# Kernel tuning notes

Measured on AMD Instinct MI355X. Metric: run time of the kernel, lower is better.

Reference implementation:

```python
import jax, jax.numpy as jnp
import numpy as np

B, N, E, H = 2, 2048, 256, 4
DK = E // H


def setup_inputs() -> dict:
    key = jax.random.key(0)
    ks = jax.random.split(key, 7)
    xav = lambda k, shape, fan_in, fan_out: jax.random.uniform(
        k, shape, minval=-1.0, maxval=1.0, dtype=jnp.float32
    ) * np.sqrt(6.0 / (fan_in + fan_out))
    return {
        "node_embeddings": jax.random.normal(ks[0], (B, N, E), dtype=jnp.float32),
        "adjacency_matrices": jax.random.randint(ks[1], (B, N, N), 0, 2, dtype=jnp.int32),
        "Wq": xav(ks[2], (H, E, DK), E, DK),
        "Wk": xav(ks[3], (H, E, DK), E, DK),
        "Wv": xav(ks[4], (H, E, DK), E, DK),
        "Wo": xav(ks[5], (E, E), E, E),
        "bo": jnp.zeros((E,), dtype=jnp.float32),
    }


def reference(node_embeddings, adjacency_matrices, Wq, Wk, Wv, Wo, bo):
    # Per-head projections: (B,N,E) x (H,E,dk) -> (B,H,N,dk)
    Q = jnp.einsum("bnd,hde->bhne", node_embeddings, Wq)
    K = jnp.einsum("bnd,hde->bhne", node_embeddings, Wk)
    V = jnp.einsum("bnd,hde->bhne", node_embeddings, Wv)
    scale = 1.0 / np.sqrt(DK).astype(np.float32)
    # (B,H,N,N) scores, adjacency-masked
    scores = jnp.einsum("bhne,bhme->bhnm", Q, K) * scale
    mask = adjacency_matrices[:, None, :, :] > 0  # (B,1,N,N) -> broadcast over H
    scores = jnp.where(mask, scores, -jnp.inf)
    attn = jax.nn.softmax(scores, axis=-1)
    heads = jnp.einsum("bhnm,bhme->bhne", attn, V)  # (B,H,N,dk)
    concat = heads.transpose(0, 2, 1, 3).reshape(node_embeddings.shape[0], node_embeddings.shape[1], E)
    return concat @ Wo.T + bo
```

## Files before the change

### kernel.cpp

```cpp
#include <hip/hip_runtime.h>
#include <hip/hip_bf16.h>
#include <math.h>

#define Bb 2
#define Nn 2048
#define Ee 256
#define Hh 4
#define DKk 64

typedef __bf16 bf16x8 __attribute__((ext_vector_type(8)));
typedef float f32x4 __attribute__((ext_vector_type(4)));

#define QSCALE 0.18033688011112042f
#define MOFF 20.0f

__global__ void __launch_bounds__(256) pack_fused(
        const int* __restrict__ adj,
        unsigned long long* __restrict__ bits,
        const float* __restrict__ x,
        const float* __restrict__ Wq,
        const float* __restrict__ Wk,
        const float* __restrict__ Wv,
        const float* __restrict__ Wo,
        __bf16* __restrict__ xb,
        __bf16* __restrict__ WB,
        __bf16* __restrict__ WoB) {
    int blk = blockIdx.x;
    int t = threadIdx.x;
    if (blk < 2048) {
        int wid = t >> 6, lane = t & 63;
        #pragma unroll
        for (int i = 0; i < 4; ++i) {
            int gid = blk * 16 + i * 4 + wid;
            int row = gid >> 3;
            int g = gid & 7;
            const int4* src = (const int4*)(adj + (size_t)row * Nn + g * 256) + lane;
            int4 v = *src;
            unsigned long long b0 = __ballot(v.x > 0);
            unsigned long long b1 = __ballot(v.y > 0);
            unsigned long long b2 = __ballot(v.z > 0);
            unsigned long long b3 = __ballot(v.w > 0);
            if (lane == 0) {
                ulonglong2* dst = (ulonglong2*)(bits + (size_t)gid * 4);
                ulonglong2 p0; p0.x = b0; p0.y = b1;
                ulonglong2 p1; p1.x = b2; p1.y = b3;
                dst[0] = p0;
                dst[1] = p1;
            }
        }
    } else {
        int b2 = blk - 2048;
        if (b2 < 1024) {
            size_t i = ((size_t)b2 * 256 + t) * 4;
            float4 v = *(const float4*)(x + i);
            __bf16 o[4] = {(__bf16)v.x, (__bf16)v.y, (__bf16)v.z, (__bf16)v.w};
            *(ushort4*)(xb + i) = *(ushort4*)o;
        } else if (b2 < 1024 + 768) {
            int row = b2 - 1024;
            int m = row >> 8, h = (row >> 6) & 3, e = row & 63;
            const float* W = (m == 0 ? Wq : (m == 1 ? Wk : Wv));
            float sc = (m == 0) ? QSCALE : 1.0f;
            WB[(size_t)row * 256 + t] = (__bf16)(W[h * 16384 + t * 64 + e] * sc);
        } else {
            int b3 = b2 - 1792;
            size_t i = ((size_t)b3 * 256 + t) * 4;
            float4 v = *(const float4*)(Wo + i);
            __bf16 o[4] = {(__bf16)v.x, (__bf16)v.y, (__bf16)v.z, (__bf16)v.w};
            *(ushort4*)(WoB + i) = *(ushort4*)o;
        }
    }
}

__global__ void __launch_bounds__(256) qkv_mfma(
        const __bf16* __restrict__ xb,
        const __bf16* __restrict__ WB,
        __bf16* __restrict__ Qb,
        __bf16* __restrict__ Kf,
        __bf16* __restrict__ Vf) {
    int blk = blockIdx.x;
    int bm = blk >> 1, half = blk & 1;
    int t = threadIdx.x;
    int wid = t >> 6, lane = t & 63, li = lane & 15, quad = lane >> 4;
    int row0 = bm * 16;

    bf16x8 a[8];
    const __bf16* ap = xb + (size_t)(row0 + li) * 256 + quad * 8;
    #pragma unroll
    for (int i = 0; i < 8; ++i) a[i] = *(const bf16x8*)(ap + i * 32);

    int b = row0 >> 11;
    int nloc = row0 & 2047;

    #pragma unroll 1
    for (int j = 0; j < 6; ++j) {
        int c0 = wid * 192 + half * 96 + j * 16;
        const __bf16* bp = WB + (size_t)(c0 + li) * 256 + quad * 8;
        f32x4 acc = (f32x4){0.f, 0.f, 0.f, 0.f};
        #pragma unroll
        for (int i = 0; i < 8; ++i) {
            bf16x8 bfrag = *(const bf16x8*)(bp + i * 32);
            acc = __builtin_amdgcn_mfma_f32_16x16x32_bf16(a[i], bfrag, acc, 0, 0, 0);
        }
        int m = c0 >> 8;
        int h = (c0 >> 6) & 3;
        int e0 = c0 & 63;
        int bh = b * 4 + h;
        if (m == 0) {
            size_t base = ((size_t)bh * Nn + nloc + quad * 4) * 64 + e0 + li;
            #pragma unroll
            for (int r = 0; r < 4; ++r) Qb[base + (size_t)r * 64] = (__bf16)acc[r];
        } else if (m == 1) {
            int e = e0 + li;
            int cp = e >> 5, ek = e & 31;
            int qA = ek >> 3, jA = ek & 7;
            int kt = nloc >> 4;
            size_t ub = (((size_t)(bh * 128 + kt)) * 2 + cp) * 512 + qA * 128 + jA;
            #pragma unroll
            for (int r = 0; r < 4; ++r) Kf[ub + (quad * 4 + r) * 8] = (__bf16)acc[r];
        } else {
            int e = e0 + li;
            int et = e >> 4, liA = e & 15;
            int key32 = nloc >> 5;
            int nnb = nloc & 16;
            size_t ub = (((size_t)(bh * 64 + key32)) * 4 + et) * 512 + liA * 8;
            #pragma unroll
            for (int r = 0; r < 4; ++r) {
                int nn = nnb + quad * 4 + r;
                Vf[ub + (nn >> 3) * 128 + (nn & 7)] = (__bf16)acc[r];
            }
        }
    }
}

__global__ void __launch_bounds__(256, 3) attn_kernel(
        const __bf16* __restrict__ Qb,
        const __bf16* __restrict__ Kf,
        const __bf16* __restrict__ Vf,
        const unsigned long long* __restrict__ bits,
        __bf16* __restrict__ heads) {
    __shared__ __align__(16) __bf16 PS[4][16][72];
    __shared__ float OL[4][16][68];
    __shared__ float lL[4][16];

    int blk = blockIdx.x;
    int bh = blk & 7, qt = blk >> 3;
    int b = bh >> 2, h = bh & 3;
    int t = threadIdx.x;
    int wid = t >> 6, lane = t & 63, li = lane & 15, quad = lane >> 4;
    int q0 = qt * 16;

    const __bf16* qp = Qb + ((size_t)bh * Nn + q0 + li) * 64 + quad * 8;
    bf16x8 qa0 = *(const bf16x8*)qp;
    bf16x8 qa1 = *(const bf16x8*)(qp + 32);

    f32x4 o[4];
    #pragma unroll
    for (int et = 0; et < 4; ++et) o[et] = (f32x4){0.f, 0.f, 0.f, 0.f};
    f32x4 ls = (f32x4){0.f, 0.f, 0.f, 0.f};

    const __bf16* Kfb = Kf + (size_t)bh * 131072;
    const __bf16* Vfb = Vf + (size_t)bh * 131072;
    int lanew = lane * 8;

    #pragma unroll 1
    for (int g = 0; g < 2; ++g) {
        int grp = wid * 2 + g;
        unsigned long long aw[4];
        #pragma unroll
        for (int r = 0; r < 4; ++r)
            aw[r] = bits[(((size_t)b * Nn + q0 + quad * 4 + r) * 8 + grp) * 4 + (li & 3)];

        #pragma unroll 1
        for (int tt = 0; tt < 4; ++tt) {
            int key64 = grp * 4 + tt;

            bf16x8 kb[4][2];
            #pragma unroll
            for (int nt = 0; nt < 4; ++nt)
                #pragma unroll
                for (int c = 0; c < 2; ++c)
                    kb[nt][c] = *(const bf16x8*)(Kfb + ((size_t)((key64 * 4 + nt) * 2 + c)) * 512 + lanew);
            bf16x8 vb[4][2];
            #pragma unroll
            for (int et = 0; et < 4; ++et)
                #pragma unroll
                for (int kc = 0; kc < 2; ++kc)
                    vb[et][kc] = *(const bf16x8*)(Vfb + ((size_t)((key64 * 2 + kc) * 4 + et)) * 512 + lanew);

            f32x4 s[4];
            __builtin_amdgcn_s_setprio(1);
            #pragma unroll
            for (int nt = 0; nt < 4; ++nt) {
                f32x4 z = (f32x4){-MOFF, -MOFF, -MOFF, -MOFF};
                z = __builtin_amdgcn_mfma_f32_16x16x32_bf16(qa0, kb[nt][0], z, 0, 0, 0);
                s[nt] = __builtin_amdgcn_mfma_f32_16x16x32_bf16(qa1, kb[nt][1], z, 0, 0, 0);
            }
            __builtin_amdgcn_s_setprio(0);

            int shb = tt * 16 + (li >> 2);
            unsigned awt[4];
            #pragma unroll
            for (int r = 0; r < 4; ++r) awt[r] = (unsigned)(aw[r] >> shb);

            #pragma unroll
            for (int nt = 0; nt < 4; ++nt) {
                #pragma unroll
                for (int r = 0; r < 4; ++r) {
                    unsigned bit = (awt[r] >> (nt * 4)) & 1u;
                    float p = bit ? __builtin_amdgcn_exp2f(s[nt][r]) : 0.f;
                    ls[r] += p;
                    PS[wid][quad * 4 + r][nt * 16 + li] = (__bf16)p;
                }
            }

            bf16x8 pa0 = *(const bf16x8*)&PS[wid][li][quad * 8];
            bf16x8 pa1 = *(const bf16x8*)&PS[wid][li][quad * 8 + 32];

            __builtin_amdgcn_s_setprio(1);
            #pragma unroll
            for (int et = 0; et < 4; ++et) {
                o[et] = __builtin_amdgcn_mfma_f32_16x16x32_bf16(pa0, vb[et][0], o[et], 0, 0, 0);
                o[et] = __builtin_amdgcn_mfma_f32_16x16x32_bf16(pa1, vb[et][1], o[et], 0, 0, 0);
            }
            __builtin_amdgcn_s_setprio(0);
        }
    }

    #pragma unroll
    for (int r = 0; r < 4; ++r) {
        float v = ls[r];
        v += __shfl_xor(v, 1, 64);
        v += __shfl_xor(v, 2, 64);
        v += __shfl_xor(v, 4, 64);
        v += __shfl_xor(v, 8, 64);
        if (li == 0) lL[wid][quad * 4 + r] = v;
        #pragma unroll
        for (int et = 0; et < 4; ++et)
            OL[wid][quad * 4 + r][et * 16 + li] = o[et][r];
    }
    __syncthreads();

    int qi = t >> 4, e0 = (t & 15) * 4;
    float l = lL[0][qi] + lL[1][qi] + lL[2][qi] + lL[3][qi];
    float inv = 1.0f / l;
    float s0 = 0.f, s1 = 0.f, s2 = 0.f, s3 = 0.f;
    #pragma unroll
    for (int w = 0; w < 4; ++w) {
        s0 += OL[w][qi][e0];
        s1 += OL[w][qi][e0 + 1];
        s2 += OL[w][qi][e0 + 2];
        s3 += OL[w][qi][e0 + 3];
    }
    __bf16 ob[4] = {(__bf16)(s0 * inv), (__bf16)(s1 * inv),
                    (__bf16)(s2 * inv), (__bf16)(s3 * inv)};
    __bf16* dst = heads + ((size_t)b * Nn + q0 + qi) * 256 + h * 64 + e0;
    *(ushort4*)dst = *(ushort4*)ob;
}

__global__ void __launch_bounds__(256) outproj_mfma(
        const __bf16* __restrict__ hb,
        const __bf16* __restrict__ WoB,
        const float* __restrict__ bo,
        float* __restrict__ out) {
    int blk = blockIdx.x;
    int bm = blk >> 1, half = blk & 1;
    int t = threadIdx.x;
    int wid = t >> 6, lane = t & 63, li = lane & 15, quad = lane >> 4;
    int row0 = bm * 16;

    bf16x8 a[8];
    const __bf16* ap = hb + (size_t)(row0 + li) * 256 + quad * 8;
    #pragma unroll
    for (int i = 0; i < 8; ++i) a[i] = *(const bf16x8*)(ap + i * 32);

    #pragma unroll 1
    for (int j = 0; j < 2; ++j) {
        int c0 = wid * 64 + half * 32 + j * 16;
        const __bf16* bp = WoB + (size_t)(c0 + li) * 256 + quad * 8;
        f32x4 acc = (f32x4){0.f, 0.f, 0.f, 0.f};
        #pragma unroll
        for (int i = 0; i < 8; ++i) {
            bf16x8 bfrag = *(const bf16x8*)(bp + i * 32);
            acc = __builtin_amdgcn_mfma_f32_16x16x32_bf16(a[i], bfrag, acc, 0, 0, 0);
        }
        int c = c0 + li;
        float bias = bo[c];
        size_t base = ((size_t)row0 + quad * 4) * 256 + c;
        #pragma unroll
        for (int r = 0; r < 4; ++r) out[base + (size_t)r * 256] = acc[r] + bias;
    }
}

extern "C" void kernel_launch(void* const* d_in, const int* in_sizes, int n_in,
                              void* d_out, int out_size, void* d_ws, size_t ws_size,
                              hipStream_t stream) {
    const float* x   = (const float*)d_in[0];
    const int*   adj = (const int*)d_in[1];
    const float* Wq  = (const float*)d_in[2];
    const float* Wk  = (const float*)d_in[3];
    const float* Wv  = (const float*)d_in[4];
    const float* Wo  = (const float*)d_in[5];
    const float* bo  = (const float*)d_in[6];
    float* out = (float*)d_out;

    char* ws = (char*)d_ws;
    const size_t MB = 1024 * 1024;
    __bf16* Qb  = (__bf16*)(ws);
    __bf16* Kf  = (__bf16*)(ws + 2 * MB);
    __bf16* Vf  = (__bf16*)(ws + 4 * MB);
    unsigned long long* bits = (unsigned long long*)(ws + 6 * MB);
    __bf16* xb  = (__bf16*)(ws + 7 * MB);
    __bf16* WB  = (__bf16*)(ws + 9 * MB);
    __bf16* WoB = (__bf16*)(ws + 9 * MB + 512 * 1024);
    __bf16* headsb = xb;

    pack_fused<<<3904, 256, 0, stream>>>(adj, bits, x, Wq, Wk, Wv, Wo, xb, WB, WoB);
    qkv_mfma<<<512, 256, 0, stream>>>(xb, WB, Qb, Kf, Vf);
    attn_kernel<<<Bb * Hh * (Nn / 16), 256, 0, stream>>>(Qb, Kf, Vf, bits, headsb);
    outproj_mfma<<<512, 256, 0, stream>>>(headsb, WoB, bo, out);
}
```

Baseline: 135.1 us.

## Process two 16-query tiles per attention block to reuse K/V loads

```diff
diff --git a/kernel.cpp b/kernel.cpp
--- a/kernel.cpp
+++ b/kernel.cpp
@@ -132,7 +132,7 @@
     }
 }
 
-__global__ void __launch_bounds__(256, 3) attn_kernel(
+__global__ void __launch_bounds__(256, 2) attn_kernel(
         const __bf16* __restrict__ Qb,
         const __bf16* __restrict__ Kf,
         const __bf16* __restrict__ Vf,
@@ -143,20 +143,28 @@
     __shared__ float lL[4][16];
 
     int blk = blockIdx.x;
-    int bh = blk & 7, qt = blk >> 3;
+    int bh = blk & 7, qp = blk >> 3;
     int b = bh >> 2, h = bh & 3;
     int t = threadIdx.x;
     int wid = t >> 6, lane = t & 63, li = lane & 15, quad = lane >> 4;
-    int q0 = qt * 16;
-
-    const __bf16* qp = Qb + ((size_t)bh * Nn + q0 + li) * 64 + quad * 8;
-    bf16x8 qa0 = *(const bf16x8*)qp;
-    bf16x8 qa1 = *(const bf16x8*)(qp + 32);
-
-    f32x4 o[4];
+    int q0 = qp * 32;
+
+    bf16x8 qa[2][2];
     #pragma unroll
-    for (int et = 0; et < 4; ++et) o[et] = (f32x4){0.f, 0.f, 0.f, 0.f};
-    f32x4 ls = (f32x4){0.f, 0.f, 0.f, 0.f};
+    for (int qq = 0; qq < 2; ++qq) {
+        const __bf16* qpp = Qb + ((size_t)bh * Nn + q0 + qq * 16 + li) * 64 + quad * 8;
+        qa[qq][0] = *(const bf16x8*)qpp;
+        qa[qq][1] = *(const bf16x8*)(qpp + 32);
+    }
+
+    f32x4 o[2][4];
+    #pragma unroll
+    for (int qq = 0; qq < 2; ++qq)
+        #pragma unroll
+        for (int et = 0; et < 4; ++et) o[qq][et] = (f32x4){0.f, 0.f, 0.f, 0.f};
+    f32x4 ls[2];
+    ls[0] = (f32x4){0.f, 0.f, 0.f, 0.f};
+    ls[1] = (f32x4){0.f, 0.f, 0.f, 0.f};
 
     const __bf16* Kfb = Kf + (size_t)bh * 131072;
     const __bf16* Vfb = Vf + (size_t)bh * 131072;
@@ -165,10 +173,12 @@
     #pragma unroll 1
     for (int g = 0; g < 2; ++g) {
         int grp = wid * 2 + g;
-        unsigned long long aw[4];
-        #pragma unroll
-        for (int r = 0; r < 4; ++r)
-            aw[r] = bits[(((size_t)b * Nn + q0 + quad * 4 + r) * 8 + grp) * 4 + (li & 3)];
+        unsigned long long aw[2][4];
+        #pragma unroll
+        for (int qq = 0; qq < 2; ++qq)
+            #pragma unroll
+            for (int r = 0; r < 4; ++r)
+                aw[qq][r] = bits[(((size_t)b * Nn + q0 + qq * 16 + quad * 4 + r) * 8 + grp) * 4 + (li & 3)];
 
         #pragma unroll 1
         for (int tt = 0; tt < 4; ++tt) {
@@ -187,74 +197,82 @@
                 for (int kc = 0; kc < 2; ++kc)
                     vb[et][kc] = *(const bf16x8*)(Vfb + ((size_t)((key64 * 2 + kc) * 4 + et)) * 512 + lanew);
 
-            f32x4 s[4];
-            __builtin_amdgcn_s_setprio(1);
-            #pragma unroll
-            for (int nt = 0; nt < 4; ++nt) {
-                f32x4 z = (f32x4){-MOFF, -MOFF, -MOFF, -MOFF};
-                z = __builtin_amdgcn_mfma_f32_16x16x32_bf16(qa0, kb[nt][0], z, 0, 0, 0);
-                s[nt] = __builtin_amdgcn_mfma_f32_16x16x32_bf16(qa1, kb[nt][1], z, 0, 0, 0);
+            int shb = tt * 16 + (li >> 2);
+
+            #pragma unroll
+            for (int qq = 0; qq < 2; ++qq) {
+                f32x4 s[4];
+                __builtin_amdgcn_s_setprio(1);
+                #pragma unroll
+                for (int nt = 0; nt < 4; ++nt) {
+                    f32x4 z = (f32x4){-MOFF, -MOFF, -MOFF, -MOFF};
+                    z = __builtin_amdgcn_mfma_f32_16x16x32_bf16(qa[qq][0], kb[nt][0], z, 0, 0, 0);
+                    s[nt] = __builtin_amdgcn_mfma_f32_16x16x32_bf16(qa[qq][1], kb[nt][1], z, 0, 0, 0);
+                }
+                __builtin_amdgcn_s_setprio(0);
+
+                unsigned awt[4];
+                #pragma unroll
+                for (int r = 0; r < 4; ++r) awt[r] = (unsigned)(aw[qq][r] >> shb);
+
+                #pragma unroll
+                for (int nt = 0; nt < 4; ++nt) {
+                    #pragma unroll
+                    for (int r = 0; r < 4; ++r) {
+                        unsigned bit = (awt[r] >> (nt * 4)) & 1u;
+                        float p = bit ? __builtin_amdgcn_exp2f(s[nt][r]) : 0.f;
+                        ls[qq][r] += p;
+                        PS[wid][quad * 4 + r][nt * 16 + li] = (__bf16)p;
+                    }
+                }
+
+                bf16x8 pa0 = *(const bf16x8*)&PS[wid][li][quad * 8];
+                bf16x8 pa1 = *(const bf16x8*)&PS[wid][li][quad * 8 + 32];
+
+                __builtin_amdgcn_s_setprio(1);
+                #pragma unroll
+                for (int et = 0; et < 4; ++et) {
+                    o[qq][et] = __builtin_amdgcn_mfma_f32_16x16x32_bf16(pa0, vb[et][0], o[qq][et], 0, 0, 0);
+                    o[qq][et] = __builtin_amdgcn_mfma_f32_16x16x32_bf16(pa1, vb[et][1], o[qq][et], 0, 0, 0);
+                }
+                __builtin_amdgcn_s_setprio(0);
             }
-            __builtin_amdgcn_s_setprio(0);
-
-            int shb = tt * 16 + (li >> 2);
-            unsigned awt[4];
-            #pragma unroll
-            for (int r = 0; r < 4; ++r) awt[r] = (unsigned)(aw[r] >> shb);
-
-            #pragma unroll
-            for (int nt = 0; nt < 4; ++nt) {
-                #pragma unroll
-                for (int r = 0; r < 4; ++r) {
-                    unsigned bit = (awt[r] >> (nt * 4)) & 1u;
-                    float p = bit ? __builtin_amdgcn_exp2f(s[nt][r]) : 0.f;
-                    ls[r] += p;
-                    PS[wid][quad * 4 + r][nt * 16 + li] = (__bf16)p;
-                }
-            }
-
-            bf16x8 pa0 = *(const bf16x8*)&PS[wid][li][quad * 8];
-            bf16x8 pa1 = *(const bf16x8*)&PS[wid][li][quad * 8 + 32];
-
-            __builtin_amdgcn_s_setprio(1);
-            #pragma unroll
-            for (int et = 0; et < 4; ++et) {
-                o[et] = __builtin_amdgcn_mfma_f32_16x16x32_bf16(pa0, vb[et][0], o[et], 0, 0, 0);
-                o[et] = __builtin_amdgcn_mfma_f32_16x16x32_bf16(pa1, vb[et][1], o[et], 0, 0, 0);
-            }
-            __builtin_amdgcn_s_setprio(0);
-        }
-    }
-
-    #pragma unroll
-    for (int r = 0; r < 4; ++r) {
-        float v = ls[r];
-        v += __shfl_xor(v, 1, 64);
-        v += __shfl_xor(v, 2, 64);
-        v += __shfl_xor(v, 4, 64);
-        v += __shfl_xor(v, 8, 64);
-        if (li == 0) lL[wid][quad * 4 + r] = v;
-        #pragma unroll
-        for (int et = 0; et < 4; ++et)
-            OL[wid][quad * 4 + r][et * 16 + li] = o[et][r];
-    }
-    __syncthreads();
-
-    int qi = t >> 4, e0 = (t & 15) * 4;
-    float l = lL[0][qi] + lL[1][qi] + lL[2][qi] + lL[3][qi];
-    float inv = 1.0f / l;
-    float s0 = 0.f, s1 = 0.f, s2 = 0.f, s3 = 0.f;
-    #pragma unroll
-    for (int w = 0; w < 4; ++w) {
-        s0 += OL[w][qi][e0];
-        s1 += OL[w][qi][e0 + 1];
-        s2 += OL[w][qi][e0 + 2];
-        s3 += OL[w][qi][e0 + 3];
-    }
-    __bf16 ob[4] = {(__bf16)(s0 * inv), (__bf16)(s1 * inv),
-                    (__bf16)(s2 * inv), (__bf16)(s3 * inv)};
-    __bf16* dst = heads + ((size_t)b * Nn + q0 + qi) * 256 + h * 64 + e0;
-    *(ushort4*)dst = *(ushort4*)ob;
+        }
+    }
+
+    #pragma unroll 1
+    for (int qq = 0; qq < 2; ++qq) {
+        #pragma unroll
+        for (int r = 0; r < 4; ++r) {
+            float v = ls[qq][r];
+            v += __shfl_xor(v, 1, 64);
+            v += __shfl_xor(v, 2, 64);
+            v += __shfl_xor(v, 4, 64);
+            v += __shfl_xor(v, 8, 64);
+            if (li == 0) lL[wid][quad * 4 + r] = v;
+            #pragma unroll
+            for (int et = 0; et < 4; ++et)
+                OL[wid][quad * 4 + r][et * 16 + li] = o[qq][et][r];
+        }
+        __syncthreads();
+
+        int qi = t >> 4, e0 = (t & 15) * 4;
+        float l = lL[0][qi] + lL[1][qi] + lL[2][qi] + lL[3][qi];
+        float inv = 1.0f / l;
+        float s0 = 0.f, s1 = 0.f, s2 = 0.f, s3 = 0.f;
+        #pragma unroll
+        for (int w = 0; w < 4; ++w) {
+            s0 += OL[w][qi][e0];
+            s1 += OL[w][qi][e0 + 1];
+            s2 += OL[w][qi][e0 + 2];
+            s3 += OL[w][qi][e0 + 3];
+        }
+        __bf16 ob[4] = {(__bf16)(s0 * inv), (__bf16)(s1 * inv),
+                        (__bf16)(s2 * inv), (__bf16)(s3 * inv)};
+        __bf16* dst = heads + ((size_t)b * Nn + q0 + qq * 16 + qi) * 256 + h * 64 + e0;
+        *(ushort4*)dst = *(ushort4*)ob;
+        __syncthreads();
+    }
 }
 
 __global__ void __launch_bounds__(256) outproj_mfma(
@@ -316,6 +334,6 @@
 
     pack_fused<<<3904, 256, 0, stream>>>(adj, bits, x, Wq, Wk, Wv, Wo, xb, WB, WoB);
     qkv_mfma<<<512, 256, 0, stream>>>(xb, WB, Qb, Kf, Vf);
-    attn_kernel<<<Bb * Hh * (Nn / 16), 256, 0, stream>>>(Qb, Kf, Vf, bits, headsb);
+    attn_kernel<<<512, 256, 0, stream>>>(Qb, Kf, Vf, bits, headsb);
     outproj_mfma<<<512, 256, 0, stream>>>(headsb, WoB, bo, out);
 }
```

After: 138.0 us. 2.1% more time.

## Fuse all four stages into one cooperative persistent kernel with grid syncs

Applied to the files above, without the earlier changes.

```diff
diff --git a/kernel.cpp b/kernel.cpp
--- a/kernel.cpp
+++ b/kernel.cpp
@@ -1,6 +1,8 @@
 #include <hip/hip_runtime.h>
+#include <hip/hip_cooperative_groups.h>
 #include <hip/hip_bf16.h>
-#include <math.h>
+
+namespace cg = cooperative_groups;
 
 #define Bb 2
 #define Nn 2048
@@ -14,7 +16,7 @@
 #define QSCALE 0.18033688011112042f
 #define MOFF 20.0f
 
-__global__ void __launch_bounds__(256) pack_fused(
+__global__ void __launch_bounds__(512) fused_all(
         const int* __restrict__ adj,
         unsigned long long* __restrict__ bits,
         const float* __restrict__ x,
@@ -22,16 +24,30 @@
         const float* __restrict__ Wk,
         const float* __restrict__ Wv,
         const float* __restrict__ Wo,
+        const float* __restrict__ bo,
         __bf16* __restrict__ xb,
         __bf16* __restrict__ WB,
-        __bf16* __restrict__ WoB) {
+        __bf16* __restrict__ WoB,
+        __bf16* __restrict__ Qb,
+        __bf16* __restrict__ Kf,
+        __bf16* __restrict__ Vf,
+        __bf16* __restrict__ heads,
+        float* __restrict__ out) {
+    cg::grid_group grid = cg::this_grid();
+
     int blk = blockIdx.x;
     int t = threadIdx.x;
-    if (blk < 2048) {
-        int wid = t >> 6, lane = t & 63;
-        #pragma unroll
-        for (int i = 0; i < 4; ++i) {
-            int gid = blk * 16 + i * 4 + wid;
+    int wid = t >> 6, lane = t & 63, li = lane & 15, quad = lane >> 4;
+    int w4 = wid & 3, sub = wid >> 2;
+
+    __shared__ __align__(16) __bf16 PS[8][16][72];
+    __shared__ float OL[8][16][68];
+    __shared__ float lL[8][16];
+
+    {
+        #pragma unroll 4
+        for (int i = 0; i < 16; ++i) {
+            int gid = blk * 128 + wid * 16 + i;
             int row = gid >> 3;
             int g = gid & 7;
             const int4* src = (const int4*)(adj + (size_t)row * Nn + g * 256) + lane;
@@ -48,246 +64,232 @@
                 dst[1] = p1;
             }
         }
-    } else {
-        int b2 = blk - 2048;
-        if (b2 < 1024) {
-            size_t i = ((size_t)b2 * 256 + t) * 4;
+        int tid = blk * 512 + t;
+        #pragma unroll
+        for (int j = 0; j < 2; ++j) {
+            size_t i = ((size_t)(tid + j * 131072)) * 4;
             float4 v = *(const float4*)(x + i);
-            __bf16 o[4] = {(__bf16)v.x, (__bf16)v.y, (__bf16)v.z, (__bf16)v.w};
-            *(ushort4*)(xb + i) = *(ushort4*)o;
-        } else if (b2 < 1024 + 768) {
-            int row = b2 - 1024;
-            int m = row >> 8, h = (row >> 6) & 3, e = row & 63;
-            const float* W = (m == 0 ? Wq : (m == 1 ? Wk : Wv));
-            float sc = (m == 0) ? QSCALE : 1.0f;
-            WB[(size_t)row * 256 + t] = (__bf16)(W[h * 16384 + t * 64 + e] * sc);
-        } else {
-            int b3 = b2 - 1792;
-            size_t i = ((size_t)b3 * 256 + t) * 4;
+            __bf16 o4[4] = {(__bf16)v.x, (__bf16)v.y, (__bf16)v.z, (__bf16)v.w};
+            *(ushort4*)(xb + i) = *(ushort4*)o4;
+        }
+        #pragma unroll
+        for (int j = 0; j < 2; ++j) {
+            int id = tid + j * 131072;
+            if (id < 196608) {
+                int row = id >> 8, col = id & 255;
+                int m = row >> 8, h = (row >> 6) & 3, e = row & 63;
+                const float* W = (m == 0 ? Wq : (m == 1 ? Wk : Wv));
+                float sc = (m == 0) ? QSCALE : 1.0f;
+                WB[(size_t)row * 256 + col] = (__bf16)(W[h * 16384 + col * 64 + e] * sc);
+            }
+        }
+        if (tid < 16384) {
+            size_t i = (size_t)tid * 4;
             float4 v = *(const float4*)(Wo + i);
-            __bf16 o[4] = {(__bf16)v.x, (__bf16)v.y, (__bf16)v.z, (__bf16)v.w};
-            *(ushort4*)(WoB + i) = *(ushort4*)o;
+            __bf16 o4[4] = {(__bf16)v.x, (__bf16)v.y, (__bf16)v.z, (__bf16)v.w};
+            *(ushort4*)(WoB + i) = *(ushort4*)o4;
         }
     }
-}
-
-__global__ void __launch_bounds__(256) qkv_mfma(
-        const __bf16* __restrict__ xb,
-        const __bf16* __restrict__ WB,
-        __bf16* __restrict__ Qb,
-        __bf16* __restrict__ Kf,
-        __bf16* __restrict__ Vf) {
-    int blk = blockIdx.x;
-    int bm = blk >> 1, half = blk & 1;
-    int t = threadIdx.x;
-    int wid = t >> 6, lane = t & 63, li = lane & 15, quad = lane >> 4;
-    int row0 = bm * 16;
-
-    bf16x8 a[8];
-    const __bf16* ap = xb + (size_t)(row0 + li) * 256 + quad * 8;
-    #pragma unroll
-    for (int i = 0; i < 8; ++i) a[i] = *(const bf16x8*)(ap + i * 32);
-
-    int b = row0 >> 11;
-    int nloc = row0 & 2047;
-
-    #pragma unroll 1
-    for (int j = 0; j < 6; ++j) {
-        int c0 = wid * 192 + half * 96 + j * 16;
-        const __bf16* bp = WB + (size_t)(c0 + li) * 256 + quad * 8;
-        f32x4 acc = (f32x4){0.f, 0.f, 0.f, 0.f};
+    __threadfence();
+    grid.sync();
+
+    {
+        int row0 = blk * 16;
+        bf16x8 a[8];
+        const __bf16* ap = xb + (size_t)(row0 + li) * 256 + quad * 8;
         #pragma unroll
-        for (int i = 0; i < 8; ++i) {
-            bf16x8 bfrag = *(const bf16x8*)(bp + i * 32);
-            acc = __builtin_amdgcn_mfma_f32_16x16x32_bf16(a[i], bfrag, acc, 0, 0, 0);
-        }
-        int m = c0 >> 8;
-        int h = (c0 >> 6) & 3;
-        int e0 = c0 & 63;
-        int bh = b * 4 + h;
-        if (m == 0) {
-            size_t base = ((size_t)bh * Nn + nloc + quad * 4) * 64 + e0 + li;
-            #pragma unroll
-            for (int r = 0; r < 4; ++r) Qb[base + (size_t)r * 64] = (__bf16)acc[r];
-        } else if (m == 1) {
-            int e = e0 + li;
-            int cp = e >> 5, ek = e & 31;
-            int qA = ek >> 3, jA = ek & 7;
-            int kt = nloc >> 4;
-            size_t ub = (((size_t)(bh * 128 + kt)) * 2 + cp) * 512 + qA * 128 + jA;
-            #pragma unroll
-            for (int r = 0; r < 4; ++r) Kf[ub + (quad * 4 + r) * 8] = (__bf16)acc[r];
-        } else {
-            int e = e0 + li;
-            int et = e >> 4, liA = e & 15;
-            int key32 = nloc >> 5;
-            int nnb = nloc & 16;
-            size_t ub = (((size_t)(bh * 64 + key32)) * 4 + et) * 512 + liA * 8;
+        for (int i = 0; i < 8; ++i) a[i] = *(const bf16x8*)(ap + i * 32);
+
+        int b = row0 >> 11;
+        int nloc = row0 & 2047;
+
+        #pragma unroll 1
+        for (int j = 0; j < 6; ++j) {
+            int c0 = w4 * 192 + sub * 96 + j * 16;
+            const __bf16* bp = WB + (size_t)(c0 + li) * 256 + quad * 8;
+            f32x4 acc = (f32x4){0.f, 0.f, 0.f, 0.f};
+            #pragma unroll
+            for (int i = 0; i < 8; ++i) {
+                bf16x8 bfrag = *(const bf16x8*)(bp + i * 32);
+                acc = __builtin_amdgcn_mfma_f32_16x16x32_bf16(a[i], bfrag, acc, 0, 0, 0);
+            }
+            int m = c0 >> 8;
+            int h = (c0 >> 6) & 3;
+            int e0 = c0 & 63;
+            int bh = b * 4 + h;
+            if (m == 0) {
+                size_t base = ((size_t)bh * Nn + nloc + quad * 4) * 64 + e0 + li;
+                #pragma unroll
+                for (int r = 0; r < 4; ++r) Qb[base + (size_t)r * 64] = (__bf16)acc[r];
+            } else if (m == 1) {
+                int e = e0 + li;
+                int cp = e >> 5, ek = e & 31;
+                int qA = ek >> 3, jA = ek & 7;
+                int kt = nloc >> 4;
+                size_t ub = (((size_t)(bh * 128 + kt)) * 2 + cp) * 512 + qA * 128 + jA;
+                #pragma unroll
+                for (int r = 0; r < 4; ++r) Kf[ub + (quad * 4 + r) * 8] = (__bf16)acc[r];
+            } else {
+                int e = e0 + li;
+                int et = e >> 4, liA = e & 15;
+                int key32 = nloc >> 5;
+                int nnb = nloc & 16;
+                size_t ub = (((size_t)(bh * 64 + key32)) * 4 + et) * 512 + liA * 8;
+                #pragma unroll
+                for (int r = 0; r < 4; ++r) {
+                    int nn = nnb + quad * 4 + r;
+                    Vf[ub + (nn >> 3) * 128 + (nn & 7)] = (__bf16)acc[r];
+                }
+            }
+        }
+    }
+    __threadfence();
+    grid.sync();
+
+    {
+        int bh = blk & 7, pp = blk >> 3;
+        int b = bh >> 2, h = bh & 3;
+        const __bf16* Kfb = Kf + (size_t)bh * 131072;
+        const __bf16* Vfb = Vf + (size_t)bh * 131072;
+        int lanew = lane * 8;
+
+        #pragma unroll 1
+        for (int qi = 0; qi < 2; ++qi) {
+            int q0 = (pp * 4 + sub * 2 + qi) * 16;
+
+            const __bf16* qp = Qb + ((size_t)bh * Nn + q0 + li) * 64 + quad * 8;
+            bf16x8 qa0 = *(const bf16x8*)qp;
+            bf16x8 qa1 = *(const bf16x8*)(qp + 32);
+
+            f32x4 o[4];
+            #pragma unroll
+            for (int et = 0; et < 4; ++et) o[et] = (f32x4){0.f, 0.f, 0.f, 0.f};
+            f32x4 ls = (f32x4){0.f, 0.f, 0.f, 0.f};
+
+            #pragma unroll 1
+            for (int g = 0; g < 2; ++g) {
+                int grp = w4 * 2 + g;
+                unsigned long long aw[4];
+                #pragma unroll
+                for (int r = 0; r < 4; ++r)
+                    aw[r] = bits[(((size_t)b * Nn + q0 + quad * 4 + r) * 8 + grp) * 4 + (li & 3)];
+
+                #pragma unroll 1
+                for (int tt = 0; tt < 4; ++tt) {
+                    int key64 = grp * 4 + tt;
+
+                    bf16x8 kb[4][2];
+                    #pragma unroll
+                    for (int nt = 0; nt < 4; ++nt)
+                        #pragma unroll
+                        for (int c = 0; c < 2; ++c)
+                            kb[nt][c] = *(const bf16x8*)(Kfb + ((size_t)((key64 * 4 + nt) * 2 + c)) * 512 + lanew);
+                    bf16x8 vb[4][2];
+                    #pragma unroll
+                    for (int et = 0; et < 4; ++et)
+                        #pragma unroll
+                        for (int kc = 0; kc < 2; ++kc)
+                            vb[et][kc] = *(const bf16x8*)(Vfb + ((size_t)((key64 * 2 + kc) * 4 + et)) * 512 + lanew);
+
+                    f32x4 s[4];
+                    __builtin_amdgcn_s_setprio(1);
+                    #pragma unroll
+                    for (int nt = 0; nt < 4; ++nt) {
+                        f32x4 z = (f32x4){-MOFF, -MOFF, -MOFF, -MOFF};
+                        z = __builtin_amdgcn_mfma_f32_16x16x32_bf16(qa0, kb[nt][0], z, 0, 0, 0);
+                        s[nt] = __builtin_amdgcn_mfma_f32_16x16x32_bf16(qa1, kb[nt][1], z, 0, 0, 0);
+                    }
+                    __builtin_amdgcn_s_setprio(0);
+
+                    int shb = tt * 16 + (li >> 2);
+                    unsigned awt[4];
+                    #pragma unroll
+                    for (int r = 0; r < 4; ++r) awt[r] = (unsigned)(aw[r] >> shb);
+
+                    #pragma unroll
+                    for (int nt = 0; nt < 4; ++nt) {
+                        #pragma unroll
+                        for (int r = 0; r < 4; ++r) {
+                            unsigned bit = (awt[r] >> (nt * 4)) & 1u;
+                            float p = bit ? __builtin_amdgcn_exp2f(s[nt][r]) : 0.f;
+                            ls[r] += p;
+                            PS[wid][quad * 4 + r][nt * 16 + li] = (__bf16)p;
+                        }
+                    }
+
+                    bf16x8 pa0 = *(const bf16x8*)&PS[wid][li][quad * 8];
+                    bf16x8 pa1 = *(const bf16x8*)&PS[wid][li][quad * 8 + 32];
+
+                    __builtin_amdgcn_s_setprio(1);
+                    #pragma unroll
+                    for (int et = 0; et < 4; ++et) {
+                        o[et] = __builtin_amdgcn_mfma_f32_16x16x32_bf16(pa0, vb[et][0], o[et], 0, 0, 0);
+                        o[et] = __builtin_amdgcn_mfma_f32_16x16x32_bf16(pa1, vb[et][1], o[et], 0, 0, 0);
+                    }
+                    __builtin_amdgcn_s_setprio(0);
+                }
+            }
+
             #pragma unroll
             for (int r = 0; r < 4; ++r) {
-                int nn = nnb + quad * 4 + r;
-                Vf[ub + (nn >> 3) * 128 + (nn & 7)] = (__bf16)acc[r];
-            }
+                float v = ls[r];
+                v += __shfl_xor(v, 1, 64);
+                v += __shfl_xor(v, 2, 64);
+                v += __shfl_xor(v, 4, 64);
+                v += __shfl_xor(v, 8, 64);
+                if (li == 0) lL[wid][quad * 4 + r] = v;
+                #pragma unroll
+                for (int et = 0; et < 4; ++et)
+                    OL[wid][quad * 4 + r][et * 16 + li] = o[et][r];
+            }
+            __syncthreads();
+
+            int tl = t & 255;
+            int qrow = tl >> 4, e0 = (tl & 15) * 4;
+            int wb0 = sub * 4;
+            float l = lL[wb0][qrow] + lL[wb0 + 1][qrow] + lL[wb0 + 2][qrow] + lL[wb0 + 3][qrow];
+            float inv = 1.0f / l;
+            float s0 = 0.f, s1 = 0.f, s2 = 0.f, s3 = 0.f;
+            #pragma unroll
+            for (int w = 0; w < 4; ++w) {
+                s0 += OL[wb0 + w][qrow][e0];
+                s1 += OL[wb0 + w][qrow][e0 + 1];
+                s2 += OL[wb0 + w][qrow][e0 + 2];
+                s3 += OL[wb0 + w][qrow][e0 + 3];
+            }
+            __bf16 ob[4] = {(__bf16)(s0 * inv), (__bf16)(s1 * inv),
+                            (__bf16)(s2 * inv), (__bf16)(s3 * inv)};
+            __bf16* dst = heads + ((size_t)b * Nn + q0 + qrow) * 256 + h * 64 + e0;
+            *(ushort4*)dst = *(ushort4*)ob;
+            __syncthreads();
         }
     }
-}
-
-__global__ void __launch_bounds__(256, 3) attn_kernel(
-        const __bf16* __restrict__ Qb,
-        const __bf16* __restrict__ Kf,
-        const __bf16* __restrict__ Vf,
-        const unsigned long long* __restrict__ bits,
-        __bf16* __restrict__ heads) {
-    __shared__ __align__(16) __bf16 PS[4][16][72];
-    __shared__ float OL[4][16][68];
-    __shared__ float lL[4][16];
-
-    int blk = blockIdx.x;
-    int bh = blk & 7, qt = blk >> 3;
-    int b = bh >> 2, h = bh & 3;
-    int t = threadIdx.x;
-    int wid = t >> 6, lane = t & 63, li = lane & 15, quad = lane >> 4;
-    int q0 = qt * 16;
-
-    const __bf16* qp = Qb + ((size_t)bh * Nn + q0 + li) * 64 + quad * 8;
-    bf16x8 qa0 = *(const bf16x8*)qp;
-    bf16x8 qa1 = *(const bf16x8*)(qp + 32);
-
-    f32x4 o[4];
-    #pragma unroll
-    for (int et = 0; et < 4; ++et) o[et] = (f32x4){0.f, 0.f, 0.f, 0.f};
-    f32x4 ls = (f32x4){0.f, 0.f, 0.f, 0.f};
-
-    const __bf16* Kfb = Kf + (size_t)bh * 131072;
-    const __bf16* Vfb = Vf + (size_t)bh * 131072;
-    int lanew = lane * 8;
-
-    #pragma unroll 1
-    for (int g = 0; g < 2; ++g) {
-        int grp = wid * 2 + g;
-        unsigned long long aw[4];
+    __threadfence();
+    grid.sync();
+
+    {
+        int row0 = blk * 16;
+        bf16x8 a[8];
+        const __bf16* ap = heads + (size_t)(row0 + li) * 256 + quad * 8;
         #pragma unroll
-        for (int r = 0; r < 4; ++r)
-            aw[r] = bits[(((size_t)b * Nn + q0 + quad * 4 + r) * 8 + grp) * 4 + (li & 3)];
+        for (int i = 0; i < 8; ++i) a[i] = *(const bf16x8*)(ap + i * 32);
 
         #pragma unroll 1
-        for (int tt = 0; tt < 4; ++tt) {
-            int key64 = grp * 4 + tt;
-
-            bf16x8 kb[4][2];
-            #pragma unroll
-            for (int nt = 0; nt < 4; ++nt)
-                #pragma unroll
-                for (int c = 0; c < 2; ++c)
-                    kb[nt][c] = *(const bf16x8*)(Kfb + ((size_t)((key64 * 4 + nt) * 2 + c)) * 512 + lanew);
-            bf16x8 vb[4][2];
-            #pragma unroll
-            for (int et = 0; et < 4; ++et)
-                #pragma unroll
-                for (int kc = 0; kc < 2; ++kc)
-                    vb[et][kc] = *(const bf16x8*)(Vfb + ((size_t)((key64 * 2 + kc) * 4 + et)) * 512 + lanew);
-
-            f32x4 s[4];
-            __builtin_amdgcn_s_setprio(1);
-            #pragma unroll
-            for (int nt = 0; nt < 4; ++nt) {
-                f32x4 z = (f32x4){-MOFF, -MOFF, -MOFF, -MOFF};
-                z = __builtin_amdgcn_mfma_f32_16x16x32_bf16(qa0, kb[nt][0], z, 0, 0, 0);
-                s[nt] = __builtin_amdgcn_mfma_f32_16x16x32_bf16(qa1, kb[nt][1], z, 0, 0, 0);
-            }
-            __builtin_amdgcn_s_setprio(0);
-
-            int shb = tt * 16 + (li >> 2);
-            unsigned awt[4];
-            #pragma unroll
-            for (int r = 0; r < 4; ++r) awt[r] = (unsigned)(aw[r] >> shb);
-
-            #pragma unroll
-            for (int nt = 0; nt < 4; ++nt) {
-                #pragma unroll
-                for (int r = 0; r < 4; ++r) {
-                    unsigned bit = (awt[r] >> (nt * 4)) & 1u;
-                    float p = bit ? __builtin_amdgcn_exp2f(s[nt][r]) : 0.f;
-                    ls[r] += p;
-                    PS[wid][quad * 4 + r][nt * 16 + li] = (__bf16)p;
-                }
-            }
-
-            bf16x8 pa0 = *(const bf16x8*)&PS[wid][li][quad * 8];
-            bf16x8 pa1 = *(const bf16x8*)&PS[wid][li][quad * 8 + 32];
-
-            __builtin_amdgcn_s_setprio(1);
-            #pragma unroll
-            for (int et = 0; et < 4; ++et) {
-                o[et] = __builtin_amdgcn_mfma_f32_16x16x32_bf16(pa0, vb[et][0], o[et], 0, 0, 0);
-                o[et] = __builtin_amdgcn_mfma_f32_16x16x32_bf16(pa1, vb[et][1], o[et], 0, 0, 0);
-            }
-            __builtin_amdgcn_s_setprio(0);
-        }
-    }
-
-    #pragma unroll
-    for (int r = 0; r < 4; ++r) {
-        float v = ls[r];
-        v += __shfl_xor(v, 1, 64);
-        v += __shfl_xor(v, 2, 64);
-        v += __shfl_xor(v, 4, 64);
-        v += __shfl_xor(v, 8, 64);
-        if (li == 0) lL[wid][quad * 4 + r] = v;
-        #pragma unroll
-        for (int et = 0; et < 4; ++et)
-            OL[wid][quad * 4 + r][et * 16 + li] = o[et][r];
-    }
-    __syncthreads();
-
-    int qi = t >> 4, e0 = (t & 15) * 4;
-    float l = lL[0][qi] + lL[1][qi] + lL[2][qi] + lL[3][qi];
-    float inv = 1.0f / l;
-    float s0 = 0.f, s1 = 0.f, s2 = 0.f, s3 = 0.f;
-    #pragma unroll
-    for (int w = 0; w < 4; ++w) {
-        s0 += OL[w][qi][e0];
-        s1 += OL[w][qi][e0 + 1];
-        s2 += OL[w][qi][e0 + 2];
-        s3 += OL[w][qi][e0 + 3];
-    }
-    __bf16 ob[4] = {(__bf16)(s0 * inv), (__bf16)(s1 * inv),
-                    (__bf16)(s2 * inv), (__bf16)(s3 * inv)};
-    __bf16* dst = heads + ((size_t)b * Nn + q0 + qi) * 256 + h * 64 + e0;
-    *(ushort4*)dst = *(ushort4*)ob;
-}
-
-__global__ void __launch_bounds__(256) outproj_mfma(
-        const __bf16* __restrict__ hb,
-        const __bf16* __restrict__ WoB,
-        const float* __restrict__ bo,
-        float* __restrict__ out) {
-    int blk = blockIdx.x;
-    int bm = blk >> 1, half = blk & 1;
-    int t = threadIdx.x;
-    int wid = t >> 6, lane = t & 63, li = lane & 15, quad = lane >> 4;
-    int row0 = bm * 16;
-
-    bf16x8 a[8];
-    const __bf16* ap = hb + (size_t)(row0 + li) * 256 + quad * 8;
-    #pragma unroll
-    for (int i = 0; i < 8; ++i) a[i] = *(const bf16x8*)(ap + i * 32);
-
-    #pragma unroll 1
-    for (int j = 0; j < 2; ++j) {
-        int c0 = wid * 64 + half * 32 + j * 16;
-        const __bf16* bp = WoB + (size_t)(c0 + li) * 256 + quad * 8;
-        f32x4 acc = (f32x4){0.f, 0.f, 0.f, 0.f};
-        #pragma unroll
-        for (int i = 0; i < 8; ++i) {
-            bf16x8 bfrag = *(const bf16x8*)(bp + i * 32);
-            acc = __builtin_amdgcn_mfma_f32_16x16x32_bf16(a[i], bfrag, acc, 0, 0, 0);
-        }
-        int c = c0 + li;
-        float bias = bo[c];
-        size_t base = ((size_t)row0 + quad * 4) * 256 + c;
-        #pragma unroll
-        for (int r = 0; r < 4; ++r) out[base + (size_t)r * 256] = acc[r] + bias;
+        for (int j = 0; j < 2; ++j) {
+            int c0 = w4 * 64 + sub * 32 + j * 16;
+            const __bf16* bp = WoB + (size_t)(c0 + li) * 256 + quad * 8;
+            f32x4 acc = (f32x4){0.f, 0.f, 0.f, 0.f};
+            #pragma unroll
+            for (int i = 0; i < 8; ++i) {
+                bf16x8 bfrag = *(const bf16x8*)(bp + i * 32);
+                acc = __builtin_amdgcn_mfma_f32_16x16x32_bf16(a[i], bfrag, acc, 0, 0, 0);
+            }
+            int c = c0 + li;
+            float bias = bo[c];
+            size_t base = ((size_t)row0 + quad * 4) * 256 + c;
+            #pragma unroll
+            for (int r = 0; r < 4; ++r) out[base + (size_t)r * 256] = acc[r] + bias;
+        }
     }
 }
 
@@ -314,8 +316,12 @@
     __bf16* WoB = (__bf16*)(ws + 9 * MB + 512 * 1024);
     __bf16* headsb = xb;
 
-    pack_fused<<<3904, 256, 0, stream>>>(adj, bits, x, Wq, Wk, Wv, Wo, xb, WB, WoB);
-    qkv_mfma<<<512, 256, 0, stream>>>(xb, WB, Qb, Kf, Vf);
-    attn_kernel<<<Bb * Hh * (Nn / 16), 256, 0, stream>>>(Qb, Kf, Vf, bits, headsb);
-    outproj_mfma<<<512, 256, 0, stream>>>(headsb, WoB, bo, out);
+    void* args[] = {
+        (void*)&adj, (void*)&bits, (void*)&x, (void*)&Wq, (void*)&Wk,
+        (void*)&Wv, (void*)&Wo, (void*)&bo, (void*)&xb, (void*)&WB,
+        (void*)&WoB, (void*)&Qb, (void*)&Kf, (void*)&Vf, (void*)&headsb,
+        (void*)&out
+    };
+    hipLaunchCooperativeKernel((const void*)fused_all, dim3(256), dim3(512),
+                               args, 0, stream);
 }
```

New measurement: 366.8 us. +171.5%, slower.
